# Optimization experiments

Hardware: AMD Instinct MI355X
Metric: run time of the kernel (lower is better)

The kernel has to match this reference:

```python
import jax, jax.numpy as jnp
import numpy as np

B, N_TOK, DIM = 4, 16384, 256
NH, NP = 8, 4
HD = DIM // NH  # 32


def setup_inputs() -> dict:
    key = jax.random.key(0)
    ks = jax.random.split(key, 6)
    s = 0.02
    x = jax.random.normal(ks[0], (B, N_TOK, DIM), jnp.float32)
    v_w = jax.random.normal(ks[1], (DIM, DIM), jnp.float32) * s
    v_b = jnp.zeros((DIM,), jnp.float32)
    aw_w = jax.random.normal(ks[2], (NH * NP, DIM), jnp.float32) * s
    aw_b = jnp.zeros((NH * NP,), jnp.float32)
    # offsets: weight init to zeros, bias init per _reset_parameters
    off_w = jnp.zeros((NH * NP * 2, DIM), jnp.float32)
    thetas = np.arange(NH, dtype=np.float64) * (2.0 * np.pi / NH)
    g = np.stack([np.cos(thetas), np.sin(thetas)], -1)
    g = g / np.abs(g).max(-1, keepdims=True)
    g = np.tile(g[:, None, :], (1, NP, 1)) * np.arange(1, NP + 1)[None, :, None]
    off_b = jnp.asarray(g.reshape(-1), jnp.float32)
    proj_w = jax.random.normal(ks[3], (DIM, DIM), jnp.float32) * s
    proj_b = jnp.zeros((DIM,), jnp.float32)
    return dict(x=x, v_w=v_w, v_b=v_b, aw_w=aw_w, aw_b=aw_b,
                off_w=off_w, off_b=off_b, proj_w=proj_w, proj_b=proj_b,
                H=128, W=128)


def _grad_scale(t, scale):
    sg = jax.lax.stop_gradient(t)
    return sg + scale * (t - sg)


def _bilinear_point_attn(v, grid, weight):
    # v: [G, H, W, D] feature maps; grid: [G, N, P, 2] pixel coords (x, y);
    # weight: [G, N, P]. Zero padding outside the map (MSDeformAttn-style).
    G, Hh, Ww, D = v.shape
    gx, gy = grid[..., 0], grid[..., 1]
    x0 = jnp.floor(gx); y0 = jnp.floor(gy)
    wx1 = gx - x0; wx0 = 1.0 - wx1
    wy1 = gy - y0; wy0 = 1.0 - wy1
    x0i = x0.astype(jnp.int32); y0i = y0.astype(jnp.int32)
    v_flat = v.reshape(G, Hh * Ww, D)

    def gather(xi, yi):
        valid = ((xi >= 0) & (xi < Ww) & (yi >= 0) & (yi < Hh))
        xi_c = jnp.clip(xi, 0, Ww - 1)
        yi_c = jnp.clip(yi, 0, Hh - 1)
        idx = (yi_c * Ww + xi_c).reshape(G, -1, 1)
        g = jnp.take_along_axis(v_flat, idx, axis=1).reshape(*xi.shape, D)
        return g * valid[..., None].astype(v.dtype)

    g00 = gather(x0i, y0i)
    g10 = gather(x0i + 1, y0i)
    g01 = gather(x0i, y0i + 1)
    g11 = gather(x0i + 1, y0i + 1)
    samp = ((wy0 * wx0)[..., None] * g00 + (wy0 * wx1)[..., None] * g10
            + (wy1 * wx0)[..., None] * g01 + (wy1 * wx1)[..., None] * g11)
    # softmax-weighted aggregation over points
    return jnp.einsum('gnpd,gnp->gnd', samp, weight)


def reference(x, v_w, v_b, aw_w, aw_b, off_w, off_b, proj_w, proj_b, H, W):
    Bb, N, C = x.shape
    # v projection -> per-head feature maps [B*nh, H, W, hd]
    v = (x @ v_w.T + v_b).reshape(Bb, N, NH, HD)
    v = v.transpose(0, 2, 1, 3).reshape(Bb * NH, H, W, HD)
    # reference points: (x=col, y=row) pixel coords, shape [1, N, 1, 2]
    mh, mw = jnp.meshgrid(jnp.arange(H, dtype=x.dtype), jnp.arange(W, dtype=x.dtype), indexing='ij')
    ref_points = jnp.stack([mw, mh], -1).reshape(1, N, 1, 2)
    # offsets [B*nh, N, P, 2]
    offsets = (x @ off_w.T + off_b).reshape(Bb, N, NH, NP, 2)
    offsets = offsets.transpose(0, 2, 1, 3, 4).reshape(Bb * NH, N, NP, 2)
    grid = _grad_scale(ref_points + offsets, 0.1)
    # attention weights [B*nh, N, P], softmax over points
    w = (x @ aw_w.T + aw_b).reshape(Bb, N, NH, NP)
    w = w.transpose(0, 2, 1, 3).reshape(Bb * NH, N, NP)
    w = jax.nn.softmax(w, axis=-1)
    out = _bilinear_point_attn(v, grid, w)  # [B*nh, N, hd]
    out = out.reshape(Bb, NH, N, HD).transpose(0, 2, 1, 3).reshape(Bb, N, C)
    return out @ proj_w.T + proj_b
```

## Files before the change

kernel.cpp:

```cpp
#include <hip/hip_runtime.h>


typedef __attribute__((ext_vector_type(8))) short bf16x8;
typedef __attribute__((ext_vector_type(4))) float f32x4;

__device__ __forceinline__ short f2bf(float f) {
  unsigned u = __float_as_uint(f);
  u = u + 0x7FFFu + ((u >> 16) & 1u);
  return (short)(u >> 16);
}
__device__ __forceinline__ float bf2f(short s) {
  return __uint_as_float(((unsigned)(unsigned short)s) << 16);
}

__device__ __forceinline__ void gload16(const void* g, void* l) {
  __builtin_amdgcn_global_load_lds(
      (const __attribute__((address_space(1))) unsigned int*)g,
      (__attribute__((address_space(3))) unsigned int*)l, 16, 0, 0);
}

__global__ __launch_bounds__(256) void k_prep(
    const float* __restrict__ v_w, const float* __restrict__ aw_w,
    const float* __restrict__ off_w, const float* __restrict__ proj_w,
    short* __restrict__ wcat, short* __restrict__ wproj)
{
  int idx = blockIdx.x * 256 + threadIdx.x;
  if (idx < 384 * 256) {
    int row = idx >> 8;
    float val = 0.f;
    if (row < 256)      val = v_w[idx];
    else if (row < 288) val = aw_w[idx - 256 * 256];
    else if (row < 352) val = off_w[idx - 288 * 256];
    wcat[idx] = f2bf(val);
  } else {
    int j = idx - 384 * 256;
    wproj[j] = f2bf(proj_w[j]);
  }
}

__global__ __launch_bounds__(256) void k_proj(
    const float* __restrict__ x, const short* __restrict__ wcat,
    const float* __restrict__ v_b, const float* __restrict__ aw_b,
    const float* __restrict__ off_b,
    unsigned short* __restrict__ vbuf,
    float* __restrict__ wts,
    float* __restrict__ offraw)
{
  __shared__ short As[64 * 64];
  __shared__ short Bs[384 * 64];
  const int tid  = threadIdx.x;
  const int wave = tid >> 6, lane = tid & 63;
  const int row0 = blockIdx.x << 6;

  const int ar  = tid >> 2;
  const int seg = tid & 3;
  const float* xg = x + (size_t)(row0 + ar) * 256 + (seg << 4);

  const int lr = lane & 15, kg = lane >> 4;
  const int cb = wave * 96;

  f32x4 acc[4][6] = {};

  for (int kt = 0; kt < 4; ++kt) {
#pragma unroll
    for (int i = 0; i < 12; ++i) {
      int fb = (wave * 12 + i) << 6;
      int f  = fb + lane;
      int r  = f >> 3, s = f & 7;
      int g  = s ^ (r & 7);
      const short* src = wcat + (size_t)r * 256 + (kt << 6) + (g << 3);
      gload16(src, &Bs[(size_t)fb << 3]);
    }
    {
      const float* ap = xg + (kt << 6);
      f32x4 fv[4];
#pragma unroll
      for (int i = 0; i < 4; ++i) fv[i] = ((const f32x4*)ap)[i];
#pragma unroll
      for (int i = 0; i < 2; ++i) {
        bf16x8 v;
#pragma unroll
        for (int j = 0; j < 4; ++j) { v[j] = f2bf(fv[2*i][j]); v[4+j] = f2bf(fv[2*i+1][j]); }
        int g = (seg << 1) + i;
        int s = g ^ (ar & 7);
        *(bf16x8*)&As[(ar << 6) + (s << 3)] = v;
      }
    }
    __syncthreads();

#pragma unroll
    for (int ks = 0; ks < 2; ++ks) {
      bf16x8 a[4], b[6];
#pragma unroll
      for (int m = 0; m < 4; ++m) {
        int r = (m << 4) + lr;
        int g = (ks << 2) + kg;
        a[m] = *(const bf16x8*)&As[(r << 6) + ((g ^ (r & 7)) << 3)];
      }
#pragma unroll
      for (int n = 0; n < 6; ++n) {
        int r = cb + (n << 4) + lr;
        int g = (ks << 2) + kg;
        b[n] = *(const bf16x8*)&Bs[(r << 6) + ((g ^ (r & 7)) << 3)];
      }
#pragma unroll
      for (int m = 0; m < 4; ++m)
#pragma unroll
        for (int n = 0; n < 6; ++n)
          acc[m][n] = __builtin_amdgcn_mfma_f32_16x16x32_bf16(a[m], b[n], acc[m][n], 0, 0, 0);
    }
    __syncthreads();
  }

#pragma unroll
  for (int n = 0; n < 6; ++n) {
    const int cbase = cb + (n << 4);
    if (cbase >= 352) continue;
#pragma unroll
    for (int m = 0; m < 4; ++m) {
#pragma unroll
      for (int j = 0; j < 4; ++j) {
        int r = row0 + (m << 4) + (kg << 2) + j;
        int b_ = r >> 14, nn = r & 16383;
        float v = acc[m][n][j];
        if (cbase < 256) {
          int c = cbase + lr;
          int h = c >> 5, d = c & 31;
          float val = v + v_b[c];
          vbuf[(((size_t)((b_ << 3) + h) << 14) + nn) * 32 + d] = (unsigned short)f2bf(val);
        } else if (cbase < 288) {
          int q = cbase - 256 + lr;
          float val = v + aw_b[q];
          float mx = fmaxf(val, __shfl_xor(val, 1));
          mx = fmaxf(mx, __shfl_xor(mx, 2));
          float e = __expf(val - mx);
          float s = e + __shfl_xor(e, 1);
          s += __shfl_xor(s, 2);
          float w = __fdividef(e, s);
          int h = q >> 2, p = q & 3;
          wts[(((size_t)((b_ << 3) + h) << 14) + nn) * 4 + p] = w;
        } else {
          int q = cbase - 288 + lr;
          int h = q >> 3, rest = q & 7;
          offraw[(((size_t)((b_ << 3) + h) << 14) + nn) * 8 + rest] = v + off_b[q];
        }
      }
    }
  }
}

__global__ __launch_bounds__(256) void k_sample(
    const unsigned short* __restrict__ vbuf, const float* __restrict__ wts,
    const float* __restrict__ offraw, unsigned short* __restrict__ attn)
{
  const int tid  = threadIdx.x;
  const int item = (blockIdx.x << 6) + (tid >> 2);
  const int q    = tid & 3;
  const int g = item >> 14, n = item & 16383;
  const float px = (float)(n & 127), py = (float)(n >> 7);

  f32x4 w4 = *(const f32x4*)(wts + (size_t)item * 4);
  const f32x4* opv = (const f32x4*)(offraw + (size_t)item * 8);
  f32x4 o0 = opv[0], o1 = opv[1];
  float wv[4]  = {w4[0], w4[1], w4[2], w4[3]};
  float oxs[4] = {o0[0], o0[2], o1[0], o1[2]};
  float oys[4] = {o0[1], o0[3], o1[1], o1[3]};

  const unsigned short* vg = vbuf + (((size_t)g) << 19) + (q << 3);
  float o[8] = {};
#pragma unroll
  for (int p = 0; p < 4; ++p) {
    float gx = px + oxs[p], gy = py + oys[p];
    float x0f = floorf(gx), y0f = floorf(gy);
    float wx1 = gx - x0f, wx0 = 1.f - wx1;
    float wy1 = gy - y0f, wy0 = 1.f - wy1;
    int x0 = (int)x0f, y0 = (int)y0f;
    bool xv0 = (unsigned)x0 < 128u, xv1 = (unsigned)(x0 + 1) < 128u;
    bool yv0 = (unsigned)y0 < 128u, yv1 = (unsigned)(y0 + 1) < 128u;
    const unsigned short* base = vg + (((y0 << 7) + x0) << 5);
    bf16x8 c00 = {}, c10 = {}, c01 = {}, c11 = {};
    if (xv0 & yv0) c00 = *(const bf16x8*)(base);
    if (xv1 & yv0) c10 = *(const bf16x8*)(base + 32);
    if (xv0 & yv1) c01 = *(const bf16x8*)(base + 4096);
    if (xv1 & yv1) c11 = *(const bf16x8*)(base + 4128);
    float w00 = wv[p] * (wy0 * wx0), w10 = wv[p] * (wy0 * wx1);
    float w01 = wv[p] * (wy1 * wx0), w11 = wv[p] * (wy1 * wx1);
#pragma unroll
    for (int j = 0; j < 8; ++j)
      o[j] += w00 * bf2f(c00[j]) + w10 * bf2f(c10[j])
            + w01 * bf2f(c01[j]) + w11 * bf2f(c11[j]);
  }
  int b_ = g >> 3, h = g & 7;
  bf16x8 pk;
#pragma unroll
  for (int j = 0; j < 8; ++j) pk[j] = f2bf(o[j]);
  *(bf16x8*)(attn + ((((size_t)b_ << 14) + n) << 8) + (h << 5) + (q << 3)) = pk;
}

__global__ __launch_bounds__(512) void k_out(
    const unsigned short* __restrict__ attn, const short* __restrict__ wproj,
    const float* __restrict__ proj_b, float* __restrict__ out)
{
  __shared__ short As[128 * 64];
  __shared__ short Bs[256 * 64];
  const int tid  = threadIdx.x;
  const int wave = tid >> 6, lane = tid & 63;
  const int row0 = blockIdx.x << 7;

  const int wr = wave >> 2, wc = wave & 3;
  const int lr = lane & 15, kg = lane >> 4;

  f32x4 acc[4][4] = {};

  for (int kt = 0; kt < 4; ++kt) {
#pragma unroll
    for (int i = 0; i < 2; ++i) {
      int fb = ((wave << 1) + i) << 6;
      int f  = fb + lane;
      int r  = f >> 3, s = f & 7;
      int g  = s ^ (r & 7);
      const short* srcA = (const short*)attn + (size_t)(row0 + r) * 256 + (kt << 6) + (g << 3);
      gload16(srcA, &As[(size_t)fb << 3]);
    }
#pragma unroll
    for (int i = 0; i < 4; ++i) {
      int fb = ((wave << 2) + i) << 6;
      int f  = fb + lane;
      int r  = f >> 3, s = f & 7;
      int g  = s ^ (r & 7);
      const short* srcB = wproj + (size_t)r * 256 + (kt << 6) + (g << 3);
      gload16(srcB, &Bs[(size_t)fb << 3]);
    }
    __syncthreads();

#pragma unroll
    for (int ks = 0; ks < 2; ++ks) {
      bf16x8 a[4], b[4];
#pragma unroll
      for (int m = 0; m < 4; ++m) {
        int r = (wr << 6) + (m << 4) + lr;
        int g = (ks << 2) + kg;
        a[m] = *(const bf16x8*)&As[(r << 6) + ((g ^ (r & 7)) << 3)];
      }
#pragma unroll
      for (int n = 0; n < 4; ++n) {
        int r = (wc << 6) + (n << 4) + lr;
        int g = (ks << 2) + kg;
        b[n] = *(const bf16x8*)&Bs[(r << 6) + ((g ^ (r & 7)) << 3)];
      }
#pragma unroll
      for (int m = 0; m < 4; ++m)
#pragma unroll
        for (int n = 0; n < 4; ++n)
          acc[m][n] = __builtin_amdgcn_mfma_f32_16x16x32_bf16(a[m], b[n], acc[m][n], 0, 0, 0);
    }
    __syncthreads();
  }

#pragma unroll
  for (int m = 0; m < 4; ++m) {
#pragma unroll
    for (int n = 0; n < 4; ++n) {
#pragma unroll
      for (int j = 0; j < 4; ++j) {
        int r = row0 + (wr << 6) + (m << 4) + (kg << 2) + j;
        int c = (wc << 6) + (n << 4) + lr;
        out[(size_t)r * 256 + c] = acc[m][n][j] + proj_b[c];
      }
    }
  }
}

extern "C" void kernel_launch(void* const* d_in, const int* in_sizes, int n_in,
                              void* d_out, int out_size, void* d_ws, size_t ws_size,
                              hipStream_t stream)
{
  const float* x      = (const float*)d_in[0];
  const float* v_w    = (const float*)d_in[1];
  const float* v_b    = (const float*)d_in[2];
  const float* aw_w   = (const float*)d_in[3];
  const float* aw_b   = (const float*)d_in[4];
  const float* off_w  = (const float*)d_in[5];
  const float* off_b  = (const float*)d_in[6];
  const float* proj_w = (const float*)d_in[7];
  const float* proj_b = (const float*)d_in[8];
  float* out = (float*)d_out;

  char* ws = (char*)d_ws;
  short* wcat   = (short*)(ws + 0);
  short* wproj  = (short*)(ws + 262144);
  float* wts    = (float*)(ws + 1048576);
  float* offraw = (float*)(ws + 9437184);
  unsigned short* attn = (unsigned short*)(ws + 26214400);
  unsigned short* vbuf = (unsigned short*)d_out;

  hipLaunchKernelGGL(k_prep,   dim3(640),   dim3(256), 0, stream,
                     v_w, aw_w, off_w, proj_w, wcat, wproj);
  hipLaunchKernelGGL(k_proj,   dim3(1024),  dim3(256), 0, stream,
                     x, wcat, v_b, aw_b, off_b, vbuf, wts, offraw);
  hipLaunchKernelGGL(k_sample, dim3(8192),  dim3(256), 0, stream,
                     vbuf, wts, offraw, attn);
  hipLaunchKernelGGL(k_out,    dim3(512),   dim3(512), 0, stream,
                     attn, wproj, proj_b, out);
}
```

Before: 282.4 us.

## Keep weight column slices resident in LDS and stream activations directly from global

Both GEMM kernels (k_proj and k_out) now load a full-K slice of the weight matrix into LDS once per block, using an XOR swizzle. They are launched on a 2D grid: column partitions by row tiles. Each wave reads its A fragments straight from global memory into registers, converting fp32 to bf16 for k_proj, instead of staging A through LDS with per-k-tile barriers. This removes the A-tile LDS round trip and the repeated synchronisation. The cost is that x is re-read once per column partition (4x for k_proj) and the A loads are uncoalesced per-lane 16-32 byte loads.

```diff
diff --git a/kernel.cpp b/kernel.cpp
--- a/kernel.cpp
+++ b/kernel.cpp
@@ -38,7 +38,7 @@
   }
 }
 
-__global__ __launch_bounds__(256) void k_proj(
+__global__ __launch_bounds__(512, 4) void k_proj(
     const float* __restrict__ x, const short* __restrict__ wcat,
     const float* __restrict__ v_b, const float* __restrict__ aw_b,
     const float* __restrict__ off_b,
@@ -46,103 +46,86 @@
     float* __restrict__ wts,
     float* __restrict__ offraw)
 {
-  __shared__ short As[64 * 64];
-  __shared__ short Bs[384 * 64];
+  __shared__ short Bs[96 * 256];
   const int tid  = threadIdx.x;
   const int wave = tid >> 6, lane = tid & 63;
-  const int row0 = blockIdx.x << 6;
-
-  const int ar  = tid >> 2;
-  const int seg = tid & 3;
-  const float* xg = x + (size_t)(row0 + ar) * 256 + (seg << 4);
+  const int cp   = blockIdx.y;
+  const int by   = blockIdx.x;
+  const int cpb  = cp * 96;
+
+#pragma unroll
+  for (int i = 0; i < 6; ++i) {
+    int f   = i * 512 + tid;
+    int col = f >> 5, s = f & 31;
+    int g   = (s & 24) | ((s & 7) ^ (col & 7));
+    const short* src = wcat + (size_t)(cpb + col) * 256 + (g << 3);
+    gload16(src, &Bs[(i * 512 + (wave << 6)) << 3]);
+  }
+  __syncthreads();
 
   const int lr = lane & 15, kg = lane >> 4;
-  const int cb = wave * 96;
-
-  f32x4 acc[4][6] = {};
-
-  for (int kt = 0; kt < 4; ++kt) {
-#pragma unroll
-    for (int i = 0; i < 12; ++i) {
-      int fb = (wave * 12 + i) << 6;
-      int f  = fb + lane;
-      int r  = f >> 3, s = f & 7;
-      int g  = s ^ (r & 7);
-      const short* src = wcat + (size_t)r * 256 + (kt << 6) + (g << 3);
-      gload16(src, &Bs[(size_t)fb << 3]);
-    }
-    {
-      const float* ap = xg + (kt << 6);
-      f32x4 fv[4];
-#pragma unroll
-      for (int i = 0; i < 4; ++i) fv[i] = ((const f32x4*)ap)[i];
-#pragma unroll
-      for (int i = 0; i < 2; ++i) {
+
+#pragma unroll
+  for (int sl = 0; sl < 2; ++sl) {
+    const int sr0 = (by << 9) + ((wave + (sl << 3)) << 5);
+    f32x4 acc[2][6] = {};
+
+#pragma unroll
+    for (int ks = 0; ks < 8; ++ks) {
+      bf16x8 a[2];
+#pragma unroll
+      for (int rf = 0; rf < 2; ++rf) {
+        const float* ap = x + (size_t)(sr0 + (rf << 4) + lr) * 256 + (ks << 5) + (kg << 3);
+        f32x4 f0 = *(const f32x4*)ap;
+        f32x4 f1 = *(const f32x4*)(ap + 4);
         bf16x8 v;
 #pragma unroll
-        for (int j = 0; j < 4; ++j) { v[j] = f2bf(fv[2*i][j]); v[4+j] = f2bf(fv[2*i+1][j]); }
-        int g = (seg << 1) + i;
-        int s = g ^ (ar & 7);
-        *(bf16x8*)&As[(ar << 6) + (s << 3)] = v;
-      }
-    }
-    __syncthreads();
-
-#pragma unroll
-    for (int ks = 0; ks < 2; ++ks) {
-      bf16x8 a[4], b[6];
-#pragma unroll
-      for (int m = 0; m < 4; ++m) {
-        int r = (m << 4) + lr;
+        for (int j = 0; j < 4; ++j) { v[j] = f2bf(f0[j]); v[4 + j] = f2bf(f1[j]); }
+        a[rf] = v;
+      }
+#pragma unroll
+      for (int cf = 0; cf < 6; ++cf) {
+        int col = (cf << 4) + lr;
         int g = (ks << 2) + kg;
-        a[m] = *(const bf16x8*)&As[(r << 6) + ((g ^ (r & 7)) << 3)];
-      }
-#pragma unroll
-      for (int n = 0; n < 6; ++n) {
-        int r = cb + (n << 4) + lr;
-        int g = (ks << 2) + kg;
-        b[n] = *(const bf16x8*)&Bs[(r << 6) + ((g ^ (r & 7)) << 3)];
-      }
-#pragma unroll
-      for (int m = 0; m < 4; ++m)
-#pragma unroll
-        for (int n = 0; n < 6; ++n)
-          acc[m][n] = __builtin_amdgcn_mfma_f32_16x16x32_bf16(a[m], b[n], acc[m][n], 0, 0, 0);
-    }
-    __syncthreads();
-  }
-
-#pragma unroll
-  for (int n = 0; n < 6; ++n) {
-    const int cbase = cb + (n << 4);
-    if (cbase >= 352) continue;
-#pragma unroll
-    for (int m = 0; m < 4; ++m) {
-#pragma unroll
-      for (int j = 0; j < 4; ++j) {
-        int r = row0 + (m << 4) + (kg << 2) + j;
-        int b_ = r >> 14, nn = r & 16383;
-        float v = acc[m][n][j];
-        if (cbase < 256) {
-          int c = cbase + lr;
-          int h = c >> 5, d = c & 31;
-          float val = v + v_b[c];
-          vbuf[(((size_t)((b_ << 3) + h) << 14) + nn) * 32 + d] = (unsigned short)f2bf(val);
-        } else if (cbase < 288) {
-          int q = cbase - 256 + lr;
-          float val = v + aw_b[q];
-          float mx = fmaxf(val, __shfl_xor(val, 1));
-          mx = fmaxf(mx, __shfl_xor(mx, 2));
-          float e = __expf(val - mx);
-          float s = e + __shfl_xor(e, 1);
-          s += __shfl_xor(s, 2);
-          float w = __fdividef(e, s);
-          int h = q >> 2, p = q & 3;
-          wts[(((size_t)((b_ << 3) + h) << 14) + nn) * 4 + p] = w;
-        } else {
-          int q = cbase - 288 + lr;
-          int h = q >> 3, rest = q & 7;
-          offraw[(((size_t)((b_ << 3) + h) << 14) + nn) * 8 + rest] = v + off_b[q];
+        int s = (g & 24) | ((g & 7) ^ (col & 7));
+        bf16x8 b = *(const bf16x8*)&Bs[(col << 8) + (s << 3)];
+        acc[0][cf] = __builtin_amdgcn_mfma_f32_16x16x32_bf16(a[0], b, acc[0][cf], 0, 0, 0);
+        acc[1][cf] = __builtin_amdgcn_mfma_f32_16x16x32_bf16(a[1], b, acc[1][cf], 0, 0, 0);
+      }
+    }
+
+#pragma unroll
+    for (int cf = 0; cf < 6; ++cf) {
+      const int cbase = cpb + (cf << 4);
+      if (cbase >= 352) continue;
+#pragma unroll
+      for (int rf = 0; rf < 2; ++rf) {
+#pragma unroll
+        for (int j = 0; j < 4; ++j) {
+          int r = sr0 + (rf << 4) + (kg << 2) + j;
+          int b_ = r >> 14, nn = r & 16383;
+          float v = acc[rf][cf][j];
+          if (cbase < 256) {
+            int c = cbase + lr;
+            int h = c >> 5, d = c & 31;
+            float val = v + v_b[c];
+            vbuf[(((size_t)((b_ << 3) + h) << 14) + nn) * 32 + d] = (unsigned short)f2bf(val);
+          } else if (cbase < 288) {
+            int q = cbase - 256 + lr;
+            float val = v + aw_b[q];
+            float mx = fmaxf(val, __shfl_xor(val, 1));
+            mx = fmaxf(mx, __shfl_xor(mx, 2));
+            float e = __expf(val - mx);
+            float ssum = e + __shfl_xor(e, 1);
+            ssum += __shfl_xor(ssum, 2);
+            float w = __fdividef(e, ssum);
+            int h = q >> 2, p = q & 3;
+            wts[(((size_t)((b_ << 3) + h) << 14) + nn) * 4 + p] = w;
+          } else {
+            int q = cbase - 288 + lr;
+            int h = q >> 3, rest = q & 7;
+            offraw[(((size_t)((b_ << 3) + h) << 14) + nn) * 8 + rest] = v + off_b[q];
+          }
         }
       }
     }
@@ -197,75 +180,59 @@
   *(bf16x8*)(attn + ((((size_t)b_ << 14) + n) << 8) + (h << 5) + (q << 3)) = pk;
 }
 
-__global__ __launch_bounds__(512) void k_out(
+__global__ __launch_bounds__(512, 4) void k_out(
     const unsigned short* __restrict__ attn, const short* __restrict__ wproj,
     const float* __restrict__ proj_b, float* __restrict__ out)
 {
-  __shared__ short As[128 * 64];
-  __shared__ short Bs[256 * 64];
+  __shared__ short Bs[128 * 256];
   const int tid  = threadIdx.x;
   const int wave = tid >> 6, lane = tid & 63;
-  const int row0 = blockIdx.x << 7;
-
-  const int wr = wave >> 2, wc = wave & 3;
+  const int cp   = blockIdx.y;
+  const int by   = blockIdx.x;
+  const int cpb  = cp << 7;
+
+#pragma unroll
+  for (int i = 0; i < 8; ++i) {
+    int f   = i * 512 + tid;
+    int col = f >> 5, s = f & 31;
+    int g   = (s & 24) | ((s & 7) ^ (col & 7));
+    const short* src = wproj + (size_t)(cpb + col) * 256 + (g << 3);
+    gload16(src, &Bs[(i * 512 + (wave << 6)) << 3]);
+  }
+  __syncthreads();
+
   const int lr = lane & 15, kg = lane >> 4;
-
-  f32x4 acc[4][4] = {};
-
-  for (int kt = 0; kt < 4; ++kt) {
-#pragma unroll
-    for (int i = 0; i < 2; ++i) {
-      int fb = ((wave << 1) + i) << 6;
-      int f  = fb + lane;
-      int r  = f >> 3, s = f & 7;
-      int g  = s ^ (r & 7);
-      const short* srcA = (const short*)attn + (size_t)(row0 + r) * 256 + (kt << 6) + (g << 3);
-      gload16(srcA, &As[(size_t)fb << 3]);
-    }
-#pragma unroll
-    for (int i = 0; i < 4; ++i) {
-      int fb = ((wave << 2) + i) << 6;
-      int f  = fb + lane;
-      int r  = f >> 3, s = f & 7;
-      int g  = s ^ (r & 7);
-      const short* srcB = wproj + (size_t)r * 256 + (kt << 6) + (g << 3);
-      gload16(srcB, &Bs[(size_t)fb << 3]);
-    }
-    __syncthreads();
-
-#pragma unroll
-    for (int ks = 0; ks < 2; ++ks) {
-      bf16x8 a[4], b[4];
-#pragma unroll
-      for (int m = 0; m < 4; ++m) {
-        int r = (wr << 6) + (m << 4) + lr;
-        int g = (ks << 2) + kg;
-        a[m] = *(const bf16x8*)&As[(r << 6) + ((g ^ (r & 7)) << 3)];
-      }
-#pragma unroll
-      for (int n = 0; n < 4; ++n) {
-        int r = (wc << 6) + (n << 4) + lr;
-        int g = (ks << 2) + kg;
-        b[n] = *(const bf16x8*)&Bs[(r << 6) + ((g ^ (r & 7)) << 3)];
-      }
-#pragma unroll
-      for (int m = 0; m < 4; ++m)
-#pragma unroll
-        for (int n = 0; n < 4; ++n)
-          acc[m][n] = __builtin_amdgcn_mfma_f32_16x16x32_bf16(a[m], b[n], acc[m][n], 0, 0, 0);
-    }
-    __syncthreads();
-  }
-
-#pragma unroll
-  for (int m = 0; m < 4; ++m) {
-#pragma unroll
-    for (int n = 0; n < 4; ++n) {
+  const int sr0 = (by << 8) + (wave << 5);
+
+  f32x4 acc[2][8] = {};
+#pragma unroll
+  for (int ks = 0; ks < 8; ++ks) {
+    bf16x8 a[2];
+#pragma unroll
+    for (int rf = 0; rf < 2; ++rf)
+      a[rf] = *(const bf16x8*)((const short*)attn +
+               (size_t)(sr0 + (rf << 4) + lr) * 256 + (ks << 5) + (kg << 3));
+#pragma unroll
+    for (int cf = 0; cf < 8; ++cf) {
+      int col = (cf << 4) + lr;
+      int g = (ks << 2) + kg;
+      int s = (g & 24) | ((g & 7) ^ (col & 7));
+      bf16x8 b = *(const bf16x8*)&Bs[(col << 8) + (s << 3)];
+      acc[0][cf] = __builtin_amdgcn_mfma_f32_16x16x32_bf16(a[0], b, acc[0][cf], 0, 0, 0);
+      acc[1][cf] = __builtin_amdgcn_mfma_f32_16x16x32_bf16(a[1], b, acc[1][cf], 0, 0, 0);
+    }
+  }
+
+#pragma unroll
+  for (int cf = 0; cf < 8; ++cf) {
+    int c = cpb + (cf << 4) + lr;
+    float pb = proj_b[c];
+#pragma unroll
+    for (int rf = 0; rf < 2; ++rf) {
 #pragma unroll
       for (int j = 0; j < 4; ++j) {
-        int r = row0 + (wr << 6) + (m << 4) + (kg << 2) + j;
-        int c = (wc << 6) + (n << 4) + lr;
-        out[(size_t)r * 256 + c] = acc[m][n][j] + proj_b[c];
+        int r = sr0 + (rf << 4) + (kg << 2) + j;
+        out[(size_t)r * 256 + c] = acc[rf][cf][j] + pb;
       }
     }
   }
@@ -294,12 +261,12 @@
   unsigned short* attn = (unsigned short*)(ws + 26214400);
   unsigned short* vbuf = (unsigned short*)d_out;
 
-  hipLaunchKernelGGL(k_prep,   dim3(640),   dim3(256), 0, stream,
+  hipLaunchKernelGGL(k_prep,   dim3(640),      dim3(256), 0, stream,
                      v_w, aw_w, off_w, proj_w, wcat, wproj);
-  hipLaunchKernelGGL(k_proj,   dim3(1024),  dim3(256), 0, stream,
+  hipLaunchKernelGGL(k_proj,   dim3(128, 4),   dim3(512), 0, stream,
                      x, wcat, v_b, aw_b, off_b, vbuf, wts, offraw);
-  hipLaunchKernelGGL(k_sample, dim3(8192),  dim3(256), 0, stream,
+  hipLaunchKernelGGL(k_sample, dim3(8192),     dim3(256), 0, stream,
                      vbuf, wts, offraw, attn);
-  hipLaunchKernelGGL(k_out,    dim3(512),   dim3(512), 0, stream,
+  hipLaunchKernelGGL(k_out,    dim3(256, 2),   dim3(512), 0, stream,
                      attn, wproj, proj_b, out);
 }
```

New measurement: 233.2 us. 1.21x faster.
